# Optimization experiments

Measured on AMD Instinct MI355X. Metric: run time of the kernel, lower is better.

Reference implementation:

```python
import jax, jax.numpy as jnp
import numpy as np

# CTC-CRF constants (bonito defaults): state_len=5, alphabet='NACGT' -> n_base=4
STATE_LEN = 5
N_BASE = 4
S = N_BASE ** STATE_LEN          # 1024 states
NZ = N_BASE + 1                  # 5 incoming transitions per state (stay + 4 moves)
C = S * NZ                       # 5120 score channels per timestep


def _make_idx():
    # idx[s] = indices into alpha (previous states) feeding state s.
    # Matches torch: cat([arange(S)[:,None], arange(S).repeat_interleave(n_base).reshape(n_base,-1).T], 1)
    a = np.arange(S)
    idx = np.concatenate([a[:, None], np.repeat(a, N_BASE).reshape(N_BASE, S).T], axis=1)
    return jnp.asarray(idx, dtype=jnp.int32)  # [S, NZ]


def setup_inputs() -> dict:
    key = jax.random.key(0)
    T, N = 2000, 32
    scores = jax.random.normal(key, (T, N, C), dtype=jnp.float32)
    return {"scores": scores}


def reference(scores) -> jnp.ndarray:
    # Faithful jax version of CTC_CRF.logZ(scores) with the Log semiring:
    #   alpha[t+1] = logsumexp(Ms[t] + alpha[t][:, idx], axis=-1)
    #   logZ = logsumexp(alpha[T] + vT, axis=1)
    T, N, _ = scores.shape
    idx = _make_idx()                      # [S, NZ] int32
    Ms = scores.reshape(T, N, S, NZ)       # [T, N, S, NZ]
    v0 = jnp.zeros((N, S), dtype=scores.dtype)  # semiring one = 0.0
    vT = jnp.zeros((N, S), dtype=scores.dtype)

    def step(alpha, Ms_t):
        # alpha: [N, S]; gather predecessors -> [N, S, NZ]; semiring mul = add; sum = logsumexp
        a_next = jax.nn.logsumexp(Ms_t + alpha[:, idx], axis=-1)
        return a_next, None

    alpha_T, _ = jax.lax.scan(step, v0, Ms)
    return jax.nn.logsumexp(alpha_T + vT, axis=1)  # [N]
```

## Files before the change

### kernel.cpp

```cpp
#include <hip/hip_runtime.h>
#include <cstdint>
#include <cstddef>


#define NB 32
#define SD 1024
#define CD 5120
#define AHEAD 24
#define CHUNK 8
#define DONE_S 0x7fffffff

typedef float f4a __attribute__((ext_vector_type(4), aligned(4)));

__device__ __forceinline__ float fexp2(float x) { return __builtin_amdgcn_exp2f(x); }
__device__ __forceinline__ float flog2(float x) { return __builtin_amdgcn_logf(x); }

template <int CTRL>
__device__ __forceinline__ float dppq(float v) {
  return __int_as_float(
      __builtin_amdgcn_update_dpp(0, __float_as_int(v), CTRL, 0xF, 0xF, true));
}

__global__ void init_prog(int* prog) {
  const int i = threadIdx.x;
  if (i < NB) prog[i * 64] = 0;
}

__global__ void __launch_bounds__(1024) ctc_logz(const float* __restrict__ scores,
                                                 float* __restrict__ out,
                                                 int* __restrict__ prog, int T) {
  __shared__ float ap[2 * SD];
  __shared__ float red[16];
  __shared__ float pad[19456];
  __shared__ int pmsg;

  const int bid = blockIdx.x;
  const int u = threadIdx.x;
  if (T < 0) { pad[u] = 1.f; out[0] = pad[u ^ 1]; }

  const size_t tstr = (size_t)NB * CD;

  if (bid >= NB) {
    const int h = bid - NB;
    const int n = h & 31;
    const int parity = h >> 5;
    const float* base = scores + (size_t)n * CD;
    float acc = 0.f;
    for (int c = parity; c * CHUNK < T; c += 2) {
      const int t0 = c * CHUNK;
      int p;
      for (;;) {
        if (u == 0)
          pmsg = __hip_atomic_load(&prog[n * 64], __ATOMIC_RELAXED,
                                   __HIP_MEMORY_SCOPE_AGENT);
        __syncthreads();
        p = pmsg;
        __syncthreads();
        if (p == DONE_S || t0 < p + AHEAD) break;
        __builtin_amdgcn_s_sleep(64);
      }
      if (p == DONE_S) break;
      if (t0 + CHUNK <= p) continue;
      if (u < 320) {
        const float* cb = base + (size_t)t0 * tstr + (size_t)u * 16;
        const int lim = (T - t0 < CHUNK) ? (T - t0) : CHUNK;
        for (int s = 0; s < lim; ++s) { acc += *cb; cb += tstr; }
      }
    }
    asm volatile("" ::"v"(acc));
    return;
  }

  const int n = bid;
  const int lane = u & 63;
  const int wid = u >> 6;
  const int p = u >> 2, c = u & 3;
  const int rdoff = (c << 8) | (p ^ (c << 3));
  const int wroff = u ^ ((u & 0x300) >> 5);

  ap[u] = 1.f; ap[SD + u] = 1.f;
  float a_cur = 1.f;
  float nLf = 0.f;
  int Lnext = 0, cacc = 0;

  const float K = 1.44269504088896340736f;
  const float LN2 = 0.69314718055994530942f;

  const float* sn = scores + (size_t)n * CD + (size_t)u * 5;
  const size_t str4 = 4 * tstr;

  auto CP = [&](int t, const f4a& qa, float qb) {
    const int rb = ((t + 1) & 1) * SD;
    const float vr = ap[rb + rdoff];
    const float R = ap[rb];
    const float p0 = dppq<0x00>(vr);
    const float p1 = dppq<0x55>(vr);
    const float p2 = dppq<0xAA>(vr);
    const float p3 = dppq<0xFF>(vr);
    float e0 = fexp2(__builtin_fmaf(qa.x, K, nLf));
    float e1 = fexp2(__builtin_fmaf(qa.y, K, nLf));
    float e2 = fexp2(__builtin_fmaf(qa.z, K, nLf));
    float e3 = fexp2(__builtin_fmaf(qa.w, K, nLf));
    float e4 = fexp2(__builtin_fmaf(qb,   K, nLf));
    float s = e0 * a_cur;
    s = __builtin_fmaf(e1, p0, s);
    s = __builtin_fmaf(e2, p1, s);
    s = __builtin_fmaf(e3, p2, s);
    s = __builtin_fmaf(e4, p3, s);
    a_cur = s;
    cacc += Lnext;
    ap[(t & 1) * SD + wroff] = s;
    const int xb = ((__float_as_int(R) >> 23) & 0xFF) - 127;
    Lnext = xb >> 2;
    nLf = (float)(-Lnext);
    if (((t & 3) == 0) && (u == 0))
      __hip_atomic_store(&prog[n * 64], t, __ATOMIC_RELAXED,
                         __HIP_MEMORY_SCOPE_AGENT);
    asm volatile("s_waitcnt lgkmcnt(0)\n\ts_barrier" ::: "memory");
  };

#define PRO(cc)                                                             \
  const float* P##cc = sn + (size_t)((cc) < T ? (cc) : T - 1) * tstr;       \
  f4a qa##cc = *(const f4a*)P##cc;                                          \
  float qb##cc = P##cc[4];                                                  \
  P##cc += str4;
  PRO(0) PRO(1) PRO(2) PRO(3)
#undef PRO

  __syncthreads();

#define RL(cc)                                                              \
  qa##cc = *(const f4a*)P##cc;                                              \
  qb##cc = P##cc[4];                                                        \
  P##cc += str4;

  int t = 0;
  for (; t + 8 <= T; t += 4) {
    CP(t + 0, qa0, qb0); RL(0)
    CP(t + 1, qa1, qb1); RL(1)
    CP(t + 2, qa2, qb2); RL(2)
    CP(t + 3, qa3, qb3); RL(3)
  }
#undef RL

#define EPI1(cc)                                                            \
  if (t + (cc) < T) {                                                       \
    CP(t + (cc), qa##cc, qb##cc);                                           \
    if (t + 4 + (cc) < T) { qa##cc = *(const f4a*)P##cc; qb##cc = P##cc[4]; }\
  }
  EPI1(0) EPI1(1) EPI1(2) EPI1(3)
#undef EPI1
  t += 4;
#define EPI2(cc) if (t + (cc) < T) CP(t + (cc), qa##cc, qb##cc);
  EPI2(0) EPI2(1) EPI2(2) EPI2(3)
#undef EPI2

  if (u == 0)
    __hip_atomic_store(&prog[n * 64], DONE_S, __ATOMIC_RELAXED,
                       __HIP_MEMORY_SCOPE_AGENT);

  float v = a_cur;
#pragma unroll
  for (int d = 1; d < 64; d <<= 1) v += __shfl_xor(v, d, 64);
  if (lane == 0) red[wid] = v;
  __syncthreads();
  if (u == 0) {
    float ssum = red[0];
#pragma unroll
    for (int i = 1; i < 16; ++i) ssum += red[i];
    out[n] = LN2 * ((float)cacc + flog2(ssum));
  }
}

extern "C" void kernel_launch(void* const* d_in, const int* in_sizes, int n_in,
                              void* d_out, int out_size, void* d_ws, size_t ws_size,
                              hipStream_t stream) {
  const float* scores = (const float*)d_in[0];
  float* out = (float*)d_out;
  int* prog = (int*)d_ws;
  const long long tot = (long long)in_sizes[0];
  const int T = (int)(tot / ((long long)NB * CD));
  init_prog<<<dim3(1), dim3(64), 0, stream>>>(prog);
  ctc_logz<<<dim3(96), dim3(1024), 0, stream>>>(scores, out, prog, T);
}
```

Measured before the change: 640.1 us.

## Offload exp to producer blocks writing fp16 ring buffer consumed by recurrence

Adds a fused kernel in which 192 producer blocks compute exp2 of the scores ahead of time and write them as fp16 into a per-batch ring buffer in workspace, signalling chunk readiness through flags. The 32 recurrence blocks then read the precomputed fp16 weights instead of raw fp32 scores, which takes the exp work off the serial critical path and halves the bytes each step loads. 32 warm-up blocks pre-touch ring slots so they are cache-resident. Per-step renormalisation now multiplies by an exact power of two derived from the exponent of R. The costs are fp16 precision loss on the weights, extra global traffic for the ring buffer, and added flag-based synchronisation.

```diff
diff --git a/kernel.cpp b/kernel.cpp
--- a/kernel.cpp
+++ b/kernel.cpp
@@ -6,14 +6,19 @@
 #define NB 32
 #define SD 1024
 #define CD 5120
+#define DONE_S 0x7fffffff
+#define NWARM 40
 #define AHEAD 24
 #define CHUNK 8
-#define DONE_S 0x7fffffff
 
 typedef float f4a __attribute__((ext_vector_type(4), aligned(4)));
+typedef unsigned short u16;
+typedef u16 us4 __attribute__((ext_vector_type(4), aligned(8)));
 
 __device__ __forceinline__ float fexp2(float x) { return __builtin_amdgcn_exp2f(x); }
 __device__ __forceinline__ float flog2(float x) { return __builtin_amdgcn_logf(x); }
+__device__ __forceinline__ u16 f2h(float f) { _Float16 h = (_Float16)f; return __builtin_bit_cast(u16, h); }
+__device__ __forceinline__ float h2f(u16 b) { return (float)__builtin_bit_cast(_Float16, b); }
 
 template <int CTRL>
 __device__ __forceinline__ float dppq(float v) {
@@ -21,12 +26,232 @@
       __builtin_amdgcn_update_dpp(0, __float_as_int(v), CTRL, 0xF, 0xF, true));
 }
 
-__global__ void init_prog(int* prog) {
+__global__ void init_ws(int* ws) {
   const int i = threadIdx.x;
-  if (i < NB) prog[i * 64] = 0;
+#pragma unroll
+  for (int k = 0; k < 6; ++k) ws[i + (k << 10)] = 0;
+  __syncthreads();
+  if (i == 0)
+    __hip_atomic_store(&ws[6144], 1, __ATOMIC_RELEASE, __HIP_MEMORY_SCOPE_AGENT);
 }
 
-__global__ void __launch_bounds__(1024) ctc_logz(const float* __restrict__ scores,
+__global__ void __launch_bounds__(1024) ctc_fused(const float* __restrict__ scores,
+                                                  float* __restrict__ out,
+                                                  int* __restrict__ ws, int T, int W) {
+  __shared__ float ap[2 * SD];
+  __shared__ float red[16];
+  __shared__ float pad[19456];
+  __shared__ int pmsg;
+
+  const int bid = blockIdx.x;
+  const int u = threadIdx.x;
+  if (T < 0) { pad[u] = 1.f; out[0] = pad[u ^ 1]; }
+
+  int* prog = ws;
+  int* flags = ws + 2048;
+  u16* EA = (u16*)((char*)ws + 65536);
+  u16* EB = EA + (size_t)32 * W * 4096;
+  const size_t tstr = (size_t)NB * CD;
+  const int wmask = W - 1;
+  const int NC = (T + 15) >> 4;
+
+  if (bid >= 64) {
+    const int h = bid - 64;
+    const int n = h & 31;
+    const int k = h >> 5;
+    u16* EAw = EA + (size_t)n * W * 4096;
+    u16* EBw = EB + (size_t)n * W * 1024;
+    const float K = 1.44269504088896340736f;
+    for (int c = k; (c << 4) < T; c += 6) {
+      const int t0 = c << 4;
+      for (;;) {
+        if (u == 0) {
+          int p = __hip_atomic_load(&prog[n << 6], __ATOMIC_RELAXED, __HIP_MEMORY_SCOPE_AGENT);
+          pmsg = (p == DONE_S) ? 2 : ((t0 + 15 < p + W) ? 1 : 0);
+        }
+        __syncthreads();
+        const int st = pmsg;
+        __syncthreads();
+        if (st == 2) return;
+        if (st == 1) break;
+        __builtin_amdgcn_s_sleep(16);
+      }
+      const float* sp = scores + (size_t)n * CD + (size_t)t0 * tstr + (size_t)u * 5;
+      const int lim = (T - t0 < 16) ? (T - t0) : 16;
+#define PEMIT(RA, RB, S)                                                     \
+  {                                                                          \
+    const int slot = (t0 + (S)) & wmask;                                     \
+    us4 o;                                                                   \
+    o.x = f2h(fexp2(RA.x * K)); o.y = f2h(fexp2(RA.y * K));                  \
+    o.z = f2h(fexp2(RA.z * K)); o.w = f2h(fexp2(RA.w * K));                  \
+    __builtin_nontemporal_store(o, (us4*)(EAw + (size_t)slot * 4096 + (u << 2))); \
+    __builtin_nontemporal_store(f2h(fexp2(RB * K)), EBw + (size_t)slot * 1024 + u); \
+  }
+      f4a ra0, ra1; float rb0, rb1;
+      ra0 = *(const f4a*)sp; rb0 = sp[4]; sp += tstr;
+      if (lim > 1) { ra1 = *(const f4a*)sp; rb1 = sp[4]; }
+      sp += tstr;
+      int s = 0;
+      for (;;) {
+        PEMIT(ra0, rb0, s);
+        if (s + 2 < lim) { ra0 = *(const f4a*)sp; rb0 = sp[4]; sp += tstr; }
+        if (++s >= lim) break;
+        PEMIT(ra1, rb1, s);
+        if (s + 2 < lim) { ra1 = *(const f4a*)sp; rb1 = sp[4]; sp += tstr; }
+        if (++s >= lim) break;
+      }
+#undef PEMIT
+      __syncthreads();
+      if (u == 0)
+        __hip_atomic_store(&flags[(n << 7) + c], 1, __ATOMIC_RELEASE, __HIP_MEMORY_SCOPE_AGENT);
+    }
+    return;
+  }
+
+  if (bid >= NB) {
+    const int n = bid - NB;
+    const char* EAb = (const char*)(EA + (size_t)n * W * 4096);
+    const char* EBb = (const char*)(EB + (size_t)n * W * 1024);
+    int acc = 0;
+    for (int cb = 0; cb < NC; ++cb) {
+      for (;;) {
+        if (u == 0) {
+          int f = __hip_atomic_load(&flags[(n << 7) + cb], __ATOMIC_RELAXED, __HIP_MEMORY_SCOPE_AGENT);
+          int p = __hip_atomic_load(&prog[n << 6], __ATOMIC_RELAXED, __HIP_MEMORY_SCOPE_AGENT);
+          pmsg = (p == DONE_S) ? 2 : ((f && ((cb << 4) < p + NWARM)) ? 1 : 0);
+        }
+        __syncthreads();
+        const int st = pmsg;
+        __syncthreads();
+        if (st == 2) goto wdone;
+        if (st == 1) break;
+        __builtin_amdgcn_s_sleep(8);
+      }
+      if ((((cb) << 4) & wmask) == 0) {
+        if (u == 0)
+          (void)__hip_atomic_load(&flags[(n << 7) + cb], __ATOMIC_ACQUIRE, __HIP_MEMORY_SCOPE_AGENT);
+        __syncthreads();
+      }
+#pragma unroll
+      for (int k = 0; k < 3; ++k) {
+        const int idx = u + (k << 10);
+        if (idx < 2048) {
+          const int st = idx >> 7, ln = idx & 127;
+          const int slot = ((cb << 4) + st) & wmask;
+          acc += *(const int*)(EAb + (size_t)slot * 8192 + ln * 64);
+        } else if (idx < 2560) {
+          const int i2 = idx - 2048;
+          const int st = i2 >> 5, ln = i2 & 31;
+          const int slot = ((cb << 4) + st) & wmask;
+          acc += *(const int*)(EBb + (size_t)slot * 2048 + ln * 64);
+        }
+      }
+    }
+  wdone:
+    asm volatile("" ::"v"(acc));
+    return;
+  }
+
+  {
+    const int n = bid;
+    const int lane = u & 63;
+    const int wid = u >> 6;
+    const int p = u >> 2, c = u & 3;
+    const int rdoff = (c << 8) | (p ^ (c << 3));
+    const int wroff = u ^ ((u & 0x300) >> 5);
+
+    ap[u] = 1.f; ap[SD + u] = 1.f;
+    float a_cur = 1.f;
+    int cacc = 0;
+    const float LN2 = 0.69314718055994530942f;
+
+    const u16* EAr = EA + (size_t)n * W * 4096;
+    const u16* EBr = EB + (size_t)n * W * 1024;
+
+    auto wait_flag = [&](int cidx, bool acq) {
+      for (;;) {
+        if (u == 0)
+          pmsg = __hip_atomic_load(&flags[(n << 7) + cidx], __ATOMIC_RELAXED, __HIP_MEMORY_SCOPE_AGENT);
+        asm volatile("s_waitcnt lgkmcnt(0)\n\ts_barrier" ::: "memory");
+        const int f = pmsg;
+        asm volatile("s_barrier" ::: "memory");
+        if (f) break;
+        __builtin_amdgcn_s_sleep(2);
+      }
+      if (acq) {
+        if (u == 0)
+          (void)__hip_atomic_load(&flags[(n << 7) + cidx], __ATOMIC_ACQUIRE, __HIP_MEMORY_SCOPE_AGENT);
+        asm volatile("s_barrier" ::: "memory");
+      }
+    };
+
+    auto LD1 = [&](int tt, us4& qa, u16& qb) {
+      const int tc = tt < T ? tt : T - 1;
+      const int slot = tc & wmask;
+      qa = *(const us4*)(EAr + (size_t)slot * 4096 + (u << 2));
+      qb = EBr[(size_t)slot * 1024 + u];
+    };
+
+    auto CP = [&](int t, const us4& qa, u16 qb) {
+      const int rb = ((t + 1) & 1) << 10;
+      const float vr = ap[rb + rdoff];
+      const float R = ap[rb];
+      const float p0 = dppq<0x00>(vr);
+      const float p1 = dppq<0x55>(vr);
+      const float p2 = dppq<0xAA>(vr);
+      const float p3 = dppq<0xFF>(vr);
+      float s = h2f(qa.x) * a_cur;
+      s = __builtin_fmaf(h2f(qa.y), p0, s);
+      s = __builtin_fmaf(h2f(qa.z), p1, s);
+      s = __builtin_fmaf(h2f(qa.w), p2, s);
+      s = __builtin_fmaf(h2f(qb),   p3, s);
+      const int eR = (__float_as_int(R) >> 23) & 0xFF;
+      cacc += eR - 127;
+      s *= __int_as_float((254 - eR) << 23);
+      a_cur = s;
+      ap[((t & 1) << 10) + wroff] = s;
+      if (((t & 3) == 0) && (u == 0))
+        __hip_atomic_store(&prog[n << 6], t, __ATOMIC_RELAXED, __HIP_MEMORY_SCOPE_AGENT);
+      asm volatile("s_waitcnt lgkmcnt(0)\n\ts_barrier" ::: "memory");
+    };
+
+    us4 qa0, qa1, qa2, qa3; u16 qb0, qb1, qb2, qb3;
+    wait_flag(0, true);
+    LD1(0, qa0, qb0); LD1(1, qa1, qb1); LD1(2, qa2, qb2); LD1(3, qa3, qb3);
+    asm volatile("s_waitcnt lgkmcnt(0)\n\ts_barrier" ::: "memory");
+
+    int t = 0;
+    for (int cb = 0; cb < NC; ++cb) {
+      if (cb + 1 < NC) {
+        const bool wrap = ((((cb + 1) << 4) & wmask) == 0);
+        wait_flag(cb + 1, wrap);
+      }
+#define STEP(SS) if (t < T) { CP(t, qa##SS, qb##SS); LD1(t + 4, qa##SS, qb##SS); ++t; }
+      STEP(0) STEP(1) STEP(2) STEP(3)
+      STEP(0) STEP(1) STEP(2) STEP(3)
+      STEP(0) STEP(1) STEP(2) STEP(3)
+      STEP(0) STEP(1) STEP(2) STEP(3)
+#undef STEP
+    }
+
+    if (u == 0)
+      __hip_atomic_store(&prog[n << 6], DONE_S, __ATOMIC_RELAXED, __HIP_MEMORY_SCOPE_AGENT);
+
+    float v = a_cur;
+#pragma unroll
+    for (int d = 1; d < 64; d <<= 1) v += __shfl_xor(v, d, 64);
+    if (lane == 0) red[wid] = v;
+    __syncthreads();
+    if (u == 0) {
+      float ssum = red[0];
+#pragma unroll
+      for (int i = 1; i < 16; ++i) ssum += red[i];
+      out[n] = LN2 * ((float)cacc + flog2(ssum));
+    }
+  }
+}
+
+__global__ void __launch_bounds__(1024) ctc_base(const float* __restrict__ scores,
                                                  float* __restrict__ out,
                                                  int* __restrict__ prog, int T) {
   __shared__ float ap[2 * SD];
@@ -37,7 +262,6 @@
   const int bid = blockIdx.x;
   const int u = threadIdx.x;
   if (T < 0) { pad[u] = 1.f; out[0] = pad[u ^ 1]; }
-
   const size_t tstr = (size_t)NB * CD;
 
   if (bid >= NB) {
@@ -51,13 +275,12 @@
       int p;
       for (;;) {
         if (u == 0)
-          pmsg = __hip_atomic_load(&prog[n * 64], __ATOMIC_RELAXED,
-                                   __HIP_MEMORY_SCOPE_AGENT);
+          pmsg = __hip_atomic_load(&prog[n * 64], __ATOMIC_RELAXED, __HIP_MEMORY_SCOPE_AGENT);
         __syncthreads();
         p = pmsg;
         __syncthreads();
         if (p == DONE_S || t0 < p + AHEAD) break;
-        __builtin_amdgcn_s_sleep(64);
+        __builtin_amdgcn_s_sleep(8);
       }
       if (p == DONE_S) break;
       if (t0 + CHUNK <= p) continue;
@@ -82,10 +305,8 @@
   float a_cur = 1.f;
   float nLf = 0.f;
   int Lnext = 0, cacc = 0;
-
   const float K = 1.44269504088896340736f;
   const float LN2 = 0.69314718055994530942f;
-
   const float* sn = scores + (size_t)n * CD + (size_t)u * 5;
   const size_t str4 = 4 * tstr;
 
@@ -114,8 +335,7 @@
     Lnext = xb >> 2;
     nLf = (float)(-Lnext);
     if (((t & 3) == 0) && (u == 0))
-      __hip_atomic_store(&prog[n * 64], t, __ATOMIC_RELAXED,
-                         __HIP_MEMORY_SCOPE_AGENT);
+      __hip_atomic_store(&prog[n * 64], t, __ATOMIC_RELAXED, __HIP_MEMORY_SCOPE_AGENT);
     asm volatile("s_waitcnt lgkmcnt(0)\n\ts_barrier" ::: "memory");
   };
 
@@ -126,14 +346,11 @@
   P##cc += str4;
   PRO(0) PRO(1) PRO(2) PRO(3)
 #undef PRO
-
   __syncthreads();
-
 #define RL(cc)                                                              \
   qa##cc = *(const f4a*)P##cc;                                              \
   qb##cc = P##cc[4];                                                        \
   P##cc += str4;
-
   int t = 0;
   for (; t + 8 <= T; t += 4) {
     CP(t + 0, qa0, qb0); RL(0)
@@ -142,7 +359,6 @@
     CP(t + 3, qa3, qb3); RL(3)
   }
 #undef RL
-
 #define EPI1(cc)                                                            \
   if (t + (cc) < T) {                                                       \
     CP(t + (cc), qa##cc, qb##cc);                                           \
@@ -156,8 +372,7 @@
 #undef EPI2
 
   if (u == 0)
-    __hip_atomic_store(&prog[n * 64], DONE_S, __ATOMIC_RELAXED,
-                       __HIP_MEMORY_SCOPE_AGENT);
+    __hip_atomic_store(&prog[n * 64], DONE_S, __ATOMIC_RELAXED, __HIP_MEMORY_SCOPE_AGENT);
 
   float v = a_cur;
 #pragma unroll
@@ -177,9 +392,19 @@
                               hipStream_t stream) {
   const float* scores = (const float*)d_in[0];
   float* out = (float*)d_out;
-  int* prog = (int*)d_ws;
+  int* ws = (int*)d_ws;
   const long long tot = (long long)in_sizes[0];
   const int T = (int)(tot / ((long long)NB * CD));
-  init_prog<<<dim3(1), dim3(64), 0, stream>>>(prog);
-  ctc_logz<<<dim3(96), dim3(1024), 0, stream>>>(scores, out, prog, T);
+
+  int W = 0;
+  for (int w = 128; w >= 32; w >>= 1) {
+    const size_t need = 65536 + (size_t)32 * w * 10240;
+    if (ws_size >= need) { W = w; break; }
+  }
+  init_ws<<<dim3(1), dim3(1024), 0, stream>>>(ws);
+  if (W >= 32 && T <= 2048 && T >= 20) {
+    ctc_fused<<<dim3(256), dim3(1024), 0, stream>>>(scores, out, ws, T, W);
+  } else {
+    ctc_base<<<dim3(96), dim3(1024), 0, stream>>>(scores, out, ws, T);
+  }
 }
```

Result: slower. 1.333 ms (+108.2%).
